# Performance work log

Measured on AMD Instinct MI355X. Metric: run time of the kernel, lower is better.

Reference implementation:

```python
import jax, jax.numpy as jnp
import numpy as np

QUANT_LIMIT = 127.0  # 2**(8-1) - 1, signed int8


def _quantize(x, amax):
    # per-tensor symmetric int8 quantization: round(clip(x * 127/amax, -127, 127))
    s = QUANT_LIMIT / amax
    return jnp.round(jnp.clip(x * s, -QUANT_LIMIT, QUANT_LIMIT))


def setup_inputs() -> dict:
    key = jax.random.key(0)
    kx, kw, kb = jax.random.split(key, 3)
    B, S, K, N = 4, 2048, 4096, 4096
    x = jax.random.normal(kx, (B, S, K), dtype=jnp.float32)
    weight = jax.random.normal(kw, (N, K), dtype=jnp.float32) * 0.03  # kaiming-ish scale
    bias = jax.random.normal(kb, (N,), dtype=jnp.float32) * 0.01
    amax = jnp.float32(4.0)     # calibrated activation amax for N(0,1)
    amax_w = jnp.float32(0.12)  # calibrated weight amax
    return {"x": x, "weight": weight, "bias": bias, "amax": amax, "amax_w": amax_w}


def reference(x, weight, bias, amax, amax_w):
    # quantize to int8
    qx = _quantize(x, amax).astype(jnp.int8)           # [B,S,K]
    qw = _quantize(weight, amax_w).astype(jnp.int8)    # [N,K]
    # int8 matmul with int32 accumulation (exact-accumulation variant of the
    # approximate-multiplier kernel)
    acc = jnp.einsum("bsk,nk->bsn", qx.astype(jnp.int32), qw.astype(jnp.int32))
    # rescale: output = acc / ((127/amax) * (127/amax_w)), then bias add
    scale = (QUANT_LIMIT / amax) * (QUANT_LIMIT / amax_w)
    out = acc.astype(jnp.float32) / scale + bias
    return out
```

## Files before the change

kernel.cpp:

```cpp
#include <hip/hip_runtime.h>
#include <hip/hip_bf16.h>
#include <stdint.h>

typedef __attribute__((ext_vector_type(4))) int i32x4;

#define QLIM 127.0f
#define BM 128
#define BN 128
#define BK 64

__device__ __forceinline__ int quant_pack4(float4 v, float s) {
    float a0 = rintf(fminf(fmaxf(v.x * s, -QLIM), QLIM));
    float a1 = rintf(fminf(fmaxf(v.y * s, -QLIM), QLIM));
    float a2 = rintf(fminf(fmaxf(v.z * s, -QLIM), QLIM));
    float a3 = rintf(fminf(fmaxf(v.w * s, -QLIM), QLIM));
    return ((int)a0 & 255) | (((int)a1 & 255) << 8) |
           (((int)a2 & 255) << 16) | (((int)a3 & 255) << 24);
}

__global__ void quantize_kernel(const float* __restrict__ in, int4* __restrict__ q,
                                const float* __restrict__ amax, long n16) {
    const float s = QLIM / amax[0];
    const long stride = (long)gridDim.x * blockDim.x;
    for (long i = (long)blockIdx.x * blockDim.x + threadIdx.x; i < n16; i += stride) {
        const float4* p = (const float4*)in + i * 4;
        float4 v0 = p[0], v1 = p[1], v2 = p[2], v3 = p[3];
        int4 r;
        r.x = quant_pack4(v0, s);
        r.y = quant_pack4(v1, s);
        r.z = quant_pack4(v2, s);
        r.w = quant_pack4(v3, s);
        q[i] = r;
    }
}

__global__ __launch_bounds__(256) void gemm_i8_kernel(
    const signed char* __restrict__ A,
    const signed char* __restrict__ B,
    const float* __restrict__ bias,
    const float* __restrict__ amax,
    const float* __restrict__ amax_w,
    float* __restrict__ C,
    int M, int N, int K)
{
    __shared__ signed char As[BM * BK];
    __shared__ signed char Bs[BN * BK];

    const int tid  = threadIdx.x;
    const int wid  = tid >> 6;
    const int lane = tid & 63;
    const int wm   = wid >> 1;
    const int wn   = wid & 1;
    const int bm   = blockIdx.y;
    const int bn   = blockIdx.x;

    const int srow = tid >> 2;
    const int scol = (tid & 3) << 4;

    const signed char* a_base = A + (size_t)(bm * BM) * K;
    const signed char* b_base = B + (size_t)(bn * BN) * K;

    const int fr = lane & 15;
    const int fk = (lane >> 4) << 4;

    i32x4 acc[4][4] = {};

    for (int k0 = 0; k0 < K; k0 += BK) {
#pragma unroll
        for (int j = 0; j < 2; ++j) {
            const signed char* ag = a_base + (size_t)(j * 64 + srow) * K + k0 + scol;
            const signed char* bg = b_base + (size_t)(j * 64 + srow) * K + k0 + scol;
            __builtin_amdgcn_global_load_lds(
                (const __attribute__((address_space(1))) void*)ag,
                (__attribute__((address_space(3))) void*)(As + j * 4096 + wid * 1024),
                16, 0, 0);
            __builtin_amdgcn_global_load_lds(
                (const __attribute__((address_space(1))) void*)bg,
                (__attribute__((address_space(3))) void*)(Bs + j * 4096 + wid * 1024),
                16, 0, 0);
        }
        __syncthreads();

        i32x4 a_frag[4], b_frag[4];
#pragma unroll
        for (int m = 0; m < 4; ++m)
            a_frag[m] = *(const i32x4*)(As + (wm * 64 + m * 16 + fr) * 64 + fk);
#pragma unroll
        for (int n = 0; n < 4; ++n)
            b_frag[n] = *(const i32x4*)(Bs + (wn * 64 + n * 16 + fr) * 64 + fk);

#pragma unroll
        for (int m = 0; m < 4; ++m)
#pragma unroll
            for (int n = 0; n < 4; ++n)
                acc[m][n] = __builtin_amdgcn_mfma_i32_16x16x64_i8(
                    a_frag[m], b_frag[n], acc[m][n], 0, 0, 0);

        __syncthreads();
    }

    const float sa  = QLIM / amax[0];
    const float sw  = QLIM / amax_w[0];
    const float inv = 1.0f / (sa * sw);
    const int row0 = bm * BM + wm * 64;
    const int col0 = bn * BN + wn * 64;
#pragma unroll
    for (int m = 0; m < 4; ++m) {
#pragma unroll
        for (int n = 0; n < 4; ++n) {
            const int colc = col0 + n * 16 + fr;
            const float bv = bias[colc];
#pragma unroll
            for (int r = 0; r < 4; ++r) {
                const int rowc = row0 + m * 16 + ((lane >> 4) << 2) + r;
                C[(size_t)rowc * N + colc] = (float)acc[m][n][r] * inv + bv;
            }
        }
    }
}

extern "C" void kernel_launch(void* const* d_in, const int* in_sizes, int n_in,
                              void* d_out, int out_size, void* d_ws, size_t ws_size,
                              hipStream_t stream) {
    const float* x      = (const float*)d_in[0];
    const float* w      = (const float*)d_in[1];
    const float* bias   = (const float*)d_in[2];
    const float* amax   = (const float*)d_in[3];
    const float* amax_w = (const float*)d_in[4];
    float* out = (float*)d_out;

    const int N = in_sizes[2];
    const int K = in_sizes[1] / N;
    const int M = in_sizes[0] / K;

    signed char* qx = (signed char*)d_ws;
    signed char* qw = qx + (size_t)M * K;

    const long nx16 = (long)M * K / 16;
    const long nw16 = (long)N * K / 16;
    quantize_kernel<<<2048, 256, 0, stream>>>(x, (int4*)qx, amax, nx16);
    quantize_kernel<<<1024, 256, 0, stream>>>(w, (int4*)qw, amax_w, nw16);

    dim3 grid(N / BN, M / BM);
    gemm_i8_kernel<<<grid, 256, 0, stream>>>(qx, qw, bias, amax, amax_w, out, M, N, K);
}
```

Baseline: 442.3 us.

## Rewrite int8 GEMM as 256x256 double-buffered 8-wave pipeline and fuse quantize kernels

Replaces the 128x128 single-buffer int8 GEMM with a 256x256 tile kernel using 512 threads and a 128KB LDS double buffer. It issues global-to-LDS loads for the next K tile while MFMAs run, uses XOR-swizzled LDS layout to reduce bank conflicts, and raises wave priority around MFMA bursts. The two quantize launches are merged into one kernel that handles x and w. This trades much larger LDS use and register pressure, which limits occupancy, for more reuse and overlap. The fused quantize now processes one float4 per thread per iteration.

New measurement: 405.9 us. 1.09x faster.

```diff
diff --git a/kernel.cpp b/kernel.cpp
--- a/kernel.cpp
+++ b/kernel.cpp
@@ -1,40 +1,49 @@
 #include <hip/hip_runtime.h>
-#include <hip/hip_bf16.h>
 #include <stdint.h>
 
 typedef __attribute__((ext_vector_type(4))) int i32x4;
 
 #define QLIM 127.0f
-#define BM 128
-#define BN 128
-#define BK 64
-
-__device__ __forceinline__ int quant_pack4(float4 v, float s) {
-    float a0 = rintf(fminf(fmaxf(v.x * s, -QLIM), QLIM));
-    float a1 = rintf(fminf(fmaxf(v.y * s, -QLIM), QLIM));
-    float a2 = rintf(fminf(fmaxf(v.z * s, -QLIM), QLIM));
-    float a3 = rintf(fminf(fmaxf(v.w * s, -QLIM), QLIM));
-    return ((int)a0 & 255) | (((int)a1 & 255) << 8) |
-           (((int)a2 & 255) << 16) | (((int)a3 & 255) << 24);
-}
-
-__global__ void quantize_kernel(const float* __restrict__ in, int4* __restrict__ q,
-                                const float* __restrict__ amax, long n16) {
-    const float s = QLIM / amax[0];
+
+__global__ __launch_bounds__(256) void quantize_fused(
+    const float4* __restrict__ x, const float4* __restrict__ w,
+    int* __restrict__ q,
+    const float* __restrict__ amax, const float* __restrict__ amax_w,
+    long nx4, long ntot4)
+{
+    const float sx = QLIM / amax[0];
+    const float sw = QLIM / amax_w[0];
     const long stride = (long)gridDim.x * blockDim.x;
-    for (long i = (long)blockIdx.x * blockDim.x + threadIdx.x; i < n16; i += stride) {
-        const float4* p = (const float4*)in + i * 4;
-        float4 v0 = p[0], v1 = p[1], v2 = p[2], v3 = p[3];
-        int4 r;
-        r.x = quant_pack4(v0, s);
-        r.y = quant_pack4(v1, s);
-        r.z = quant_pack4(v2, s);
-        r.w = quant_pack4(v3, s);
-        q[i] = r;
+    for (long i = (long)blockIdx.x * blockDim.x + threadIdx.x; i < ntot4; i += stride) {
+        const bool isx = i < nx4;
+        const float4 v = isx ? x[i] : w[i - nx4];
+        const float s  = isx ? sx : sw;
+        float a0 = rintf(fminf(fmaxf(v.x * s, -QLIM), QLIM));
+        float a1 = rintf(fminf(fmaxf(v.y * s, -QLIM), QLIM));
+        float a2 = rintf(fminf(fmaxf(v.z * s, -QLIM), QLIM));
+        float a3 = rintf(fminf(fmaxf(v.w * s, -QLIM), QLIM));
+        q[i] = ((int)a0 & 255) | (((int)a1 & 255) << 8) |
+               (((int)a2 & 255) << 16) | (((int)a3 & 255) << 24);
     }
 }
 
-__global__ __launch_bounds__(256) void gemm_i8_kernel(
+
+#define STAGE(mat, tt, kh) do {                                              \
+    if ((tt) < nt) {                                                         \
+        const size_t go = (size_t)((tt) * 128 + (kh) * 64);                  \
+        const int ld = ((((tt) & 1) << 15) | ((kh) << 14));                  \
+        __builtin_amdgcn_global_load_lds(                                    \
+            (const __attribute__((address_space(1))) void*)(mat##Src + go),  \
+            (__attribute__((address_space(3))) void*)(lds + mat##Dst + ld),  \
+            16, 0, 0);                                                       \
+        __builtin_amdgcn_global_load_lds(                                    \
+            (const __attribute__((address_space(1))) void*)(mat##Src + go + rowStep), \
+            (__attribute__((address_space(3))) void*)(lds + mat##Dst + ld + 8192),    \
+            16, 0, 0);                                                       \
+    }                                                                        \
+} while (0)
+
+__global__ __launch_bounds__(512, 2) void gemm_i8_8phase(
     const signed char* __restrict__ A,
     const signed char* __restrict__ B,
     const float* __restrict__ bias,
@@ -43,76 +52,128 @@
     float* __restrict__ C,
     int M, int N, int K)
 {
-    __shared__ signed char As[BM * BK];
-    __shared__ signed char Bs[BN * BK];
+    __shared__ signed char lds[131072];
 
     const int tid  = threadIdx.x;
     const int wid  = tid >> 6;
     const int lane = tid & 63;
-    const int wm   = wid >> 1;
-    const int wn   = wid & 1;
+    const int wr   = wid >> 2;
+    const int wc   = wid & 3;
+    const int bn   = blockIdx.x;
     const int bm   = blockIdx.y;
-    const int bn   = blockIdx.x;
+    const int nt   = K >> 7;
+
+    const int fr   = lane & 15;
+    const int fk   = (lane >> 4) << 4;
+    const int fswz = ((fr >> 1) & 3) << 4;
+
+    const int aRd = (wr * 128 + fr) * 64 + (fk ^ fswz);
+    const int bRd = 65536 + (wc * 64 + fr) * 64 + (fk ^ fswz);
 
     const int srow = tid >> 2;
-    const int scol = (tid & 3) << 4;
-
-    const signed char* a_base = A + (size_t)(bm * BM) * K;
-    const signed char* b_base = B + (size_t)(bn * BN) * K;
-
-    const int fr = lane & 15;
-    const int fk = (lane >> 4) << 4;
-
-    i32x4 acc[4][4] = {};
-
-    for (int k0 = 0; k0 < K; k0 += BK) {
-#pragma unroll
-        for (int j = 0; j < 2; ++j) {
-            const signed char* ag = a_base + (size_t)(j * 64 + srow) * K + k0 + scol;
-            const signed char* bg = b_base + (size_t)(j * 64 + srow) * K + k0 + scol;
-            __builtin_amdgcn_global_load_lds(
-                (const __attribute__((address_space(1))) void*)ag,
-                (__attribute__((address_space(3))) void*)(As + j * 4096 + wid * 1024),
-                16, 0, 0);
-            __builtin_amdgcn_global_load_lds(
-                (const __attribute__((address_space(1))) void*)bg,
-                (__attribute__((address_space(3))) void*)(Bs + j * 4096 + wid * 1024),
-                16, 0, 0);
-        }
-        __syncthreads();
-
-        i32x4 a_frag[4], b_frag[4];
-#pragma unroll
-        for (int m = 0; m < 4; ++m)
-            a_frag[m] = *(const i32x4*)(As + (wm * 64 + m * 16 + fr) * 64 + fk);
-#pragma unroll
-        for (int n = 0; n < 4; ++n)
-            b_frag[n] = *(const i32x4*)(Bs + (wn * 64 + n * 16 + fr) * 64 + fk);
-
-#pragma unroll
-        for (int m = 0; m < 4; ++m)
-#pragma unroll
-            for (int n = 0; n < 4; ++n)
-                acc[m][n] = __builtin_amdgcn_mfma_i32_16x16x64_i8(
-                    a_frag[m], b_frag[n], acc[m][n], 0, 0, 0);
-
-        __syncthreads();
+    const int csw  = (((tid & 3) ^ ((tid >> 3) & 3)) << 4);
+    const signed char* aSrc = A + (size_t)(bm * 256 + srow) * K + csw;
+    const signed char* bSrc = B + (size_t)(bn * 256 + srow) * K + csw;
+    const size_t rowStep = (size_t)128 * K;
+    const int aDst = wid << 10;
+    const int bDst = 65536 + (wid << 10);
+
+    i32x4 acc[8][4] = {};
+
+    STAGE(a, 0, 0); STAGE(b, 0, 0); STAGE(a, 0, 1); STAGE(b, 0, 1);
+    STAGE(a, 1, 0); STAGE(b, 1, 0);
+    asm volatile("s_waitcnt vmcnt(4)" ::: "memory");
+    __builtin_amdgcn_s_barrier();
+
+#pragma unroll 1
+    for (int t = 0; t < nt; ++t) {
+        const int bb = (t & 1) << 15;
+        const signed char* pa = lds + bb + aRd;
+        const signed char* pb = lds + bb + bRd;
+        i32x4 af[4], bf[4];
+
+#pragma unroll
+        for (int mm = 0; mm < 4; ++mm) af[mm] = *(const i32x4*)(pa + mm * 1024);
+#pragma unroll
+        for (int nn = 0; nn < 4; ++nn) bf[nn] = *(const i32x4*)(pb + nn * 1024);
+        STAGE(a, t + 1, 1);
+        __builtin_amdgcn_s_barrier();
+        asm volatile("s_waitcnt lgkmcnt(0)" ::: "memory");
+        __builtin_amdgcn_sched_barrier(0);
+        __builtin_amdgcn_s_setprio(1);
+#pragma unroll
+        for (int mm = 0; mm < 4; ++mm)
+#pragma unroll
+            for (int nn = 0; nn < 4; ++nn)
+                acc[mm][nn] = __builtin_amdgcn_mfma_i32_16x16x64_i8(af[mm], bf[nn], acc[mm][nn], 0, 0, 0);
+        __builtin_amdgcn_s_setprio(0);
+        __builtin_amdgcn_s_barrier();
+
+#pragma unroll
+        for (int mm = 0; mm < 4; ++mm) af[mm] = *(const i32x4*)(pa + 4096 + mm * 1024);
+        STAGE(b, t + 1, 1);
+        __builtin_amdgcn_s_barrier();
+        asm volatile("s_waitcnt lgkmcnt(0)" ::: "memory");
+        __builtin_amdgcn_sched_barrier(0);
+        __builtin_amdgcn_s_setprio(1);
+#pragma unroll
+        for (int mm = 0; mm < 4; ++mm)
+#pragma unroll
+            for (int nn = 0; nn < 4; ++nn)
+                acc[4 + mm][nn] = __builtin_amdgcn_mfma_i32_16x16x64_i8(af[mm], bf[nn], acc[4 + mm][nn], 0, 0, 0);
+        __builtin_amdgcn_s_setprio(0);
+        __builtin_amdgcn_s_barrier();
+
+#pragma unroll
+        for (int mm = 0; mm < 4; ++mm) af[mm] = *(const i32x4*)(pa + 16384 + mm * 1024);
+#pragma unroll
+        for (int nn = 0; nn < 4; ++nn) bf[nn] = *(const i32x4*)(pb + 16384 + nn * 1024);
+        STAGE(a, t + 2, 0);
+        __builtin_amdgcn_s_barrier();
+        asm volatile("s_waitcnt lgkmcnt(0)" ::: "memory");
+        __builtin_amdgcn_sched_barrier(0);
+        __builtin_amdgcn_s_setprio(1);
+#pragma unroll
+        for (int mm = 0; mm < 4; ++mm)
+#pragma unroll
+            for (int nn = 0; nn < 4; ++nn)
+                acc[mm][nn] = __builtin_amdgcn_mfma_i32_16x16x64_i8(af[mm], bf[nn], acc[mm][nn], 0, 0, 0);
+        __builtin_amdgcn_s_setprio(0);
+        __builtin_amdgcn_s_barrier();
+
+#pragma unroll
+        for (int mm = 0; mm < 4; ++mm) af[mm] = *(const i32x4*)(pa + 16384 + 4096 + mm * 1024);
+        STAGE(b, t + 2, 0);
+        __builtin_amdgcn_s_barrier();
+        asm volatile("s_waitcnt lgkmcnt(0)" ::: "memory");
+        __builtin_amdgcn_sched_barrier(0);
+        __builtin_amdgcn_s_setprio(1);
+#pragma unroll
+        for (int mm = 0; mm < 4; ++mm)
+#pragma unroll
+            for (int nn = 0; nn < 4; ++nn)
+                acc[4 + mm][nn] = __builtin_amdgcn_mfma_i32_16x16x64_i8(af[mm], bf[nn], acc[4 + mm][nn], 0, 0, 0);
+        __builtin_amdgcn_s_setprio(0);
+        if (t < nt - 2) asm volatile("s_waitcnt vmcnt(4)" ::: "memory");
+        else            asm volatile("s_waitcnt vmcnt(0)" ::: "memory");
+        __builtin_amdgcn_s_barrier();
     }
 
     const float sa  = QLIM / amax[0];
     const float sw  = QLIM / amax_w[0];
     const float inv = 1.0f / (sa * sw);
-    const int row0 = bm * BM + wm * 64;
-    const int col0 = bn * BN + wn * 64;
-#pragma unroll
-    for (int m = 0; m < 4; ++m) {
+    const int row0 = bm * 256 + wr * 128;
+    const int col0 = bn * 256 + wc * 64;
+    const int rsub = (lane >> 4) << 2;
+#pragma unroll
+    for (int m = 0; m < 8; ++m) {
 #pragma unroll
         for (int n = 0; n < 4; ++n) {
             const int colc = col0 + n * 16 + fr;
             const float bv = bias[colc];
 #pragma unroll
             for (int r = 0; r < 4; ++r) {
-                const int rowc = row0 + m * 16 + ((lane >> 4) << 2) + r;
+                const int rowc = row0 + m * 16 + rsub + r;
                 C[(size_t)rowc * N + colc] = (float)acc[m][n][r] * inv + bv;
             }
         }
@@ -136,11 +197,11 @@
     signed char* qx = (signed char*)d_ws;
     signed char* qw = qx + (size_t)M * K;
 
-    const long nx16 = (long)M * K / 16;
-    const long nw16 = (long)N * K / 16;
-    quantize_kernel<<<2048, 256, 0, stream>>>(x, (int4*)qx, amax, nx16);
-    quantize_kernel<<<1024, 256, 0, stream>>>(w, (int4*)qw, amax_w, nw16);
-
-    dim3 grid(N / BN, M / BM);
-    gemm_i8_kernel<<<grid, 256, 0, stream>>>(qx, qw, bias, amax, amax_w, out, M, N, K);
+    const long nx4   = (long)M * K / 4;
+    const long ntot4 = nx4 + (long)N * K / 4;
+    quantize_fused<<<2048, 256, 0, stream>>>((const float4*)x, (const float4*)w,
+                                             (int*)qx, amax, amax_w, nx4, ntot4);
+
+    dim3 grid(N / 256, M / 256);
+    gemm_i8_8phase<<<grid, 512, 0, stream>>>(qx, qw, bias, amax, amax_w, out, M, N, K);
 }
```
